# Kernel optimization log

Measured on AMD Instinct MI355X. Metric: run time of the kernel, lower is better.

The kernel has to match this reference:

```python
import jax, jax.numpy as jnp
import numpy as np

N = 100000
E = 1600000
D_IN = 128
D_HID = 128


def setup_inputs() -> dict:
    key = jax.random.key(0)
    ks = jax.random.split(key, 10)
    x = jax.random.normal(ks[0], (N, D_IN), dtype=jnp.float32)
    edge_index = jax.random.randint(ks[1], (2, E), 0, N, dtype=jnp.int64)
    def lin(k, i, o):
        kw, kb = jax.random.split(k)
        s = 1.0 / np.sqrt(i)
        return (jax.random.uniform(kw, (o, i), jnp.float32, -s, s),
                jax.random.uniform(kb, (o,), jnp.float32, -s, s))
    w0a, b0a = lin(ks[2], D_IN, D_HID)
    w0b, b0b = lin(ks[3], D_HID, D_HID)
    w1a, b1a = lin(ks[4], D_HID, D_HID)
    w1b, b1b = lin(ks[5], D_HID, D_HID)
    return {"x": x, "edge_index": edge_index,
            "w0a": w0a, "b0a": b0a, "w0b": w0b, "b0b": b0b,
            "w1a": w1a, "b1a": b1a, "w1b": w1b, "b1b": b1b}


def _gin_layer(x, src, dst, wa, ba, wb, bb):
    # GINConv, eps=0: h_i = x_i + sum_{j in N(i)} x_j (messages from src aggregated at dst)
    agg = jax.ops.segment_sum(x[src], dst, num_segments=N)  # [N, D]
    h = x + agg
    h = jax.nn.relu(h @ wa.T + ba)  # LinearBlock (no bn, no dropout)
    return h @ wb.T + bb            # final Linear of local_nn


def reference(x, edge_index, w0a, b0a, w0b, b0b, w1a, b1a, w1b, b1b):
    src, dst = edge_index[0], edge_index[1]
    h = _gin_layer(x, src, dst, w0a, b0a, w0b, b0b)
    h = _gin_layer(h, src, dst, w1a, b1a, w1b, b1b)
    return h
```

## Files before the change

### kernel.cpp

```cpp
#include <hip/hip_runtime.h>


typedef __attribute__((ext_vector_type(8))) short bf16x8;
typedef __attribute__((ext_vector_type(4))) float floatx4;

#define WS_ALIGN(x) (((x) + 255) & ~(size_t)255)
#define NBMAX 400
#define BCAP 6144

__device__ __forceinline__ unsigned short f2b(float f) {
  unsigned u = __builtin_bit_cast(unsigned, f);
  u = (u + 0x7FFF + ((u >> 16) & 1)) >> 16;
  return (unsigned short)u;
}
__device__ __forceinline__ float b2f(unsigned u16) {
  return __builtin_bit_cast(float, u16 << 16);
}

__global__ __launch_bounds__(256) void bucket_split(const int* __restrict__ src,
                                                    const int* __restrict__ dst,
                                                    int* __restrict__ bcnt,
                                                    unsigned* __restrict__ barr, int E, int nb) {
  __shared__ int cnt[NBMAX], base[NBMAX], cur[NBMAX];
  int t = threadIdx.x;
  for (int i = t; i < nb; i += 256) { cnt[i] = 0; cur[i] = 0; }
  __syncthreads();
  int e0 = blockIdx.x * 8192;
  int s[32], d[32];
#pragma unroll
  for (int k = 0; k < 32; k++) {
    int e = e0 + k * 256 + t;
    if (e < E) { s[k] = src[e]; d[k] = dst[e]; } else { d[k] = -1; }
  }
#pragma unroll
  for (int k = 0; k < 32; k++)
    if (d[k] >= 0) atomicAdd(&cnt[d[k] >> 8], 1);
  __syncthreads();
  for (int i = t; i < nb; i += 256) base[i] = cnt[i] ? atomicAdd(&bcnt[i], cnt[i]) : 0;
  __syncthreads();
#pragma unroll
  for (int k = 0; k < 32; k++)
    if (d[k] >= 0) {
      int b = d[k] >> 8;
      int r = atomicAdd(&cur[b], 1);
      barr[(size_t)b * BCAP + base[b] + r] = ((unsigned)(d[k] & 255) << 17) | (unsigned)s[k];
    }
}

__global__ void bucket_scan(const int* __restrict__ bcnt, int* __restrict__ sbase, int nb,
                            int* __restrict__ rowptr, int n) {
  __shared__ int buf[512];
  int t = threadIdx.x;
  int v = (t < nb) ? bcnt[t] : 0;
  buf[t] = v;
  __syncthreads();
  for (int off = 1; off < 512; off <<= 1) {
    int add = (t >= off) ? buf[t - off] : 0;
    __syncthreads();
    buf[t] += add;
    __syncthreads();
  }
  if (t < nb) sbase[t] = buf[t] - v;
  if (t == nb - 1) { sbase[nb] = buf[t]; rowptr[n] = buf[t]; }
}

__global__ __launch_bounds__(256) void bucket_csr(const unsigned* __restrict__ barr,
                                                  const int* __restrict__ bcnt,
                                                  const int* __restrict__ sbase,
                                                  int* __restrict__ rowptr, int* __restrict__ srt,
                                                  int n) {
  __shared__ int cnt[256], off[256], off2[256];
  int b = blockIdx.x, t = threadIdx.x;
  int cb = bcnt[b];
  int node0 = b * 256;
  int nlocal = min(256, n - node0);
  cnt[t] = 0;
  off2[t] = 0;
  __syncthreads();
  const unsigned* bp = barr + (size_t)b * BCAP;
  for (int i = t; i < cb; i += 256) atomicAdd(&cnt[bp[i] >> 17], 1);
  __syncthreads();
  int v = cnt[t];
  off[t] = v;
  __syncthreads();
  for (int o = 1; o < 256; o <<= 1) {
    int add = (t >= o) ? off[t - o] : 0;
    __syncthreads();
    off[t] += add;
    __syncthreads();
  }
  int excl = off[t] - v;
  int sb = sbase[b];
  if (t < nlocal) rowptr[node0 + t] = sb + excl;
  cnt[t] = excl;
  __syncthreads();
  for (int i = t; i < cb; i += 256) {
    unsigned pk = bp[i];
    int local = pk >> 17;
    int r = atomicAdd(&off2[local], 1);
    srt[sb + cnt[local] + r] = pk & 0x1FFFF;
  }
}

__global__ void cvt_kernel(const float* __restrict__ x, unsigned short* __restrict__ xb, int n4) {
  int i = blockIdx.x * blockDim.x + threadIdx.x;
  if (i < n4) {
    float4 v = ((const float4*)x)[i];
    uint2 pk;
    pk.x = (unsigned)f2b(v.x) | ((unsigned)f2b(v.y) << 16);
    pk.y = (unsigned)f2b(v.z) | ((unsigned)f2b(v.w) << 16);
    ((uint2*)xb)[i] = pk;
  }
}

__global__ __launch_bounds__(256) void aggregate_bf16(const unsigned short* __restrict__ X,
                                                      const int* __restrict__ rowptr,
                                                      const int* __restrict__ srt,
                                                      unsigned short* __restrict__ out, int n) {
  int w = blockIdx.x * 4 + (threadIdx.x >> 6);
  if (w >= n) return;
  int lane = threadIdx.x & 63;
  int c = lane & 15;
  int s = lane >> 4;
  const uint4* Xv = (const uint4*)X;

  float acc[8];
#pragma unroll
  for (int i = 0; i < 8; i++) acc[i] = 0.f;

  if (s == 0) {
    uint4 u = Xv[(size_t)w * 16 + c];
    acc[0] += b2f(u.x & 0xffff); acc[1] += b2f(u.x >> 16);
    acc[2] += b2f(u.y & 0xffff); acc[3] += b2f(u.y >> 16);
    acc[4] += b2f(u.z & 0xffff); acc[5] += b2f(u.z >> 16);
    acc[6] += b2f(u.w & 0xffff); acc[7] += b2f(u.w >> 16);
  }

  int p0 = rowptr[w], e = rowptr[w + 1];
  int trips = (e - p0 + 3) >> 2;
  int idx = p0 + s;
#pragma unroll 2
  for (int i = 0; i < trips; i++, idx += 4) {
    bool valid = idx < e;
    int r = srt[valid ? idx : (e - 1)];
    uint4 u = Xv[(size_t)r * 16 + c];
    if (!valid) { u.x = 0; u.y = 0; u.z = 0; u.w = 0; }
    acc[0] += b2f(u.x & 0xffff); acc[1] += b2f(u.x >> 16);
    acc[2] += b2f(u.y & 0xffff); acc[3] += b2f(u.y >> 16);
    acc[4] += b2f(u.z & 0xffff); acc[5] += b2f(u.z >> 16);
    acc[6] += b2f(u.w & 0xffff); acc[7] += b2f(u.w >> 16);
  }

#pragma unroll
  for (int i = 0; i < 8; i++) {
    acc[i] += __shfl_xor(acc[i], 16, 64);
    acc[i] += __shfl_xor(acc[i], 32, 64);
  }

  unsigned pk = (unsigned)f2b(acc[2 * s]) | ((unsigned)f2b(acc[2 * s + 1]) << 16);
  ((unsigned*)out)[(size_t)w * 64 + c * 4 + s] = pk;
}

__device__ __forceinline__ void stage_w(char* buf, const float* __restrict__ W, int t) {
  for (int idx = t; idx < 2048; idx += 512) {
    int nrow = idx >> 4, c = idx & 15;
    float4 a = ((const float4*)W)[idx * 2];
    float4 b = ((const float4*)W)[idx * 2 + 1];
    uint4 pk;
    pk.x = (unsigned)f2b(a.x) | ((unsigned)f2b(a.y) << 16);
    pk.y = (unsigned)f2b(a.z) | ((unsigned)f2b(a.w) << 16);
    pk.z = (unsigned)f2b(b.x) | ((unsigned)f2b(b.y) << 16);
    pk.w = (unsigned)f2b(b.z) | ((unsigned)f2b(b.w) << 16);
    *(uint4*)(buf + nrow * 256 + ((c ^ (nrow & 15)) << 4)) = pk;
  }
}

template <int OUT_BF16>
__global__ __launch_bounds__(512) void mlp_kernel(
    const unsigned short* __restrict__ A, const float* __restrict__ Wa,
    const float* __restrict__ ba, const float* __restrict__ Wb,
    const float* __restrict__ bb, void* __restrict__ Cout, int n) {
  __shared__ __align__(16) char lds[65536];
  char* bufA = lds;
  char* bufB = lds + 32768;
  int t = threadIdx.x;
  stage_w(bufA, Wa, t);
  stage_w(bufB, Wb, t);

  int wave = t >> 6, lane = t & 63;
  int m = lane & 15, q = lane >> 4;
  int rbase = blockIdx.x * 128;
  int rowA = rbase + wave * 16 + m;
  int rA = rowA < n ? rowA : (n - 1);

  bf16x8 af[4];
  const bf16x8* Arow = (const bf16x8*)(A + (size_t)rA * 128);
#pragma unroll
  for (int ks = 0; ks < 4; ks++) af[ks] = Arow[ks * 4 + q];

  __syncthreads();

  floatx4 acc[8];
  floatx4 zf = {0.f, 0.f, 0.f, 0.f};
#pragma unroll
  for (int j = 0; j < 8; j++) acc[j] = zf;
#pragma unroll
  for (int ks = 0; ks < 4; ks++) {
#pragma unroll
    for (int j = 0; j < 8; j++) {
      bf16x8 bf = *(const bf16x8*)(bufA + (j * 16 + m) * 256 + (((ks * 4 + q) ^ m) << 4));
      acc[j] = __builtin_amdgcn_mfma_f32_16x16x32_bf16(af[ks], bf, acc[j], 0, 0, 0);
    }
  }
  __syncthreads();

#pragma unroll
  for (int j = 0; j < 8; j++) {
    float bias = ba[j * 16 + m];
#pragma unroll
    for (int reg = 0; reg < 4; reg++) {
      float v = fmaxf(acc[j][reg] + bias, 0.f);
      int lr = wave * 16 + q * 4 + reg;
      int col = j * 16 + m;
      *(unsigned short*)(bufA + lr * 256 + (((col >> 3) ^ (lr & 15)) << 4) + (col & 7) * 2) =
          f2b(v);
    }
  }
  __syncthreads();

  int lrA = wave * 16 + m;
#pragma unroll
  for (int ks = 0; ks < 4; ks++)
    af[ks] = *(const bf16x8*)(bufA + lrA * 256 + (((ks * 4 + q) ^ m) << 4));
#pragma unroll
  for (int j = 0; j < 8; j++) acc[j] = zf;
#pragma unroll
  for (int ks = 0; ks < 4; ks++) {
#pragma unroll
    for (int j = 0; j < 8; j++) {
      bf16x8 bf = *(const bf16x8*)(bufB + (j * 16 + m) * 256 + (((ks * 4 + q) ^ m) << 4));
      acc[j] = __builtin_amdgcn_mfma_f32_16x16x32_bf16(af[ks], bf, acc[j], 0, 0, 0);
    }
  }

#pragma unroll
  for (int j = 0; j < 8; j++) {
    float bias = bb[j * 16 + m];
#pragma unroll
    for (int reg = 0; reg < 4; reg++) {
      int row = rbase + wave * 16 + q * 4 + reg;
      if (row >= n) continue;
      float v = acc[j][reg] + bias;
      int col = j * 16 + m;
      if (OUT_BF16)
        ((unsigned short*)Cout)[(size_t)row * 128 + col] = f2b(v);
      else
        ((float*)Cout)[(size_t)row * 128 + col] = v;
    }
  }
}

extern "C" void kernel_launch(void* const* d_in, const int* in_sizes, int n_in,
                              void* d_out, int out_size, void* d_ws, size_t ws_size,
                              hipStream_t stream) {
  const float* x   = (const float*)d_in[0];
  const int*   ei  = (const int*)d_in[1];
  const float* w0a = (const float*)d_in[2];
  const float* b0a = (const float*)d_in[3];
  const float* w0b = (const float*)d_in[4];
  const float* b0b = (const float*)d_in[5];
  const float* w1a = (const float*)d_in[6];
  const float* b1a = (const float*)d_in[7];
  const float* w1b = (const float*)d_in[8];
  const float* b1b = (const float*)d_in[9];
  float* out = (float*)d_out;

  int n = in_sizes[0] / 128;
  int E = in_sizes[1] / 2;
  const int* src = ei;
  const int* dst = ei + E;
  int nb = (n + 255) / 256;

  char* w = (char*)d_ws;
  int* rowptr = (int*)w;           w += WS_ALIGN((size_t)(n + 1) * 4);
  int* sbase = (int*)w;            w += WS_ALIGN((size_t)(NBMAX + 1) * 4);
  int* bcnt = (int*)w;             w += WS_ALIGN((size_t)NBMAX * 4);
  int* srt = (int*)w;              w += WS_ALIGN((size_t)E * 4);
  unsigned short* xb = (unsigned short*)w;  w += WS_ALIGN((size_t)n * 128 * 2);
  unsigned* barr = (unsigned*)w;
  unsigned short* B1 = (unsigned short*)w;

  hipMemsetAsync(bcnt, 0, (size_t)nb * 4, stream);
  bucket_split<<<(E + 8191) / 8192, 256, 0, stream>>>(src, dst, bcnt, barr, E, nb);
  bucket_scan<<<1, 512, 0, stream>>>(bcnt, sbase, nb, rowptr, n);
  bucket_csr<<<nb, 256, 0, stream>>>(barr, bcnt, sbase, rowptr, srt, n);

  cvt_kernel<<<(n * 32 + 255) / 256, 256, 0, stream>>>(x, xb, n * 32);

  int agg_grid = (n + 3) / 4;
  int mlp_grid = (n + 127) / 128;

  aggregate_bf16<<<agg_grid, 256, 0, stream>>>(xb, rowptr, srt, B1, n);
  mlp_kernel<1><<<mlp_grid, 512, 0, stream>>>(B1, w0a, b0a, w0b, b0b, xb, n);

  aggregate_bf16<<<agg_grid, 256, 0, stream>>>(xb, rowptr, srt, B1, n);
  mlp_kernel<0><<<mlp_grid, 512, 0, stream>>>(B1, w1a, b1a, w1b, b1b, out, n);
}
```

Before: 333.5 us.

## Pre-convert weights once, read B from global, and streamline CSR build and aggregation

```diff
diff --git a/kernel.cpp b/kernel.cpp
--- a/kernel.cpp
+++ b/kernel.cpp
@@ -21,29 +21,40 @@
                                                     const int* __restrict__ dst,
                                                     int* __restrict__ bcnt,
                                                     unsigned* __restrict__ barr, int E, int nb) {
-  __shared__ int cnt[NBMAX], base[NBMAX], cur[NBMAX];
+  __shared__ int cnt[NBMAX], base[NBMAX];
   int t = threadIdx.x;
-  for (int i = t; i < nb; i += 256) { cnt[i] = 0; cur[i] = 0; }
-  __syncthreads();
-  int e0 = blockIdx.x * 8192;
-  int s[32], d[32];
-#pragma unroll
-  for (int k = 0; k < 32; k++) {
-    int e = e0 + k * 256 + t;
-    if (e < E) { s[k] = src[e]; d[k] = dst[e]; } else { d[k] = -1; }
-  }
-#pragma unroll
-  for (int k = 0; k < 32; k++)
-    if (d[k] >= 0) atomicAdd(&cnt[d[k] >> 8], 1);
+  for (int i = t; i < nb; i += 256) cnt[i] = 0;
+  __syncthreads();
+  int q0 = blockIdx.x * 1024;
+  int E4 = E >> 2;
+  int s[16], d[16];
+#pragma unroll
+  for (int r = 0; r < 4; r++) {
+    int qi = q0 + r * 256 + t;
+    if (qi < E4) {
+      int4 sv = ((const int4*)src)[qi];
+      int4 dv = ((const int4*)dst)[qi];
+      s[r * 4 + 0] = sv.x; d[r * 4 + 0] = dv.x;
+      s[r * 4 + 1] = sv.y; d[r * 4 + 1] = dv.y;
+      s[r * 4 + 2] = sv.z; d[r * 4 + 2] = dv.z;
+      s[r * 4 + 3] = sv.w; d[r * 4 + 3] = dv.w;
+    } else {
+      d[r * 4 + 0] = d[r * 4 + 1] = d[r * 4 + 2] = d[r * 4 + 3] = -1;
+    }
+  }
+  int rank[16];
+#pragma unroll
+  for (int k = 0; k < 16; k++)
+    rank[k] = (d[k] >= 0) ? atomicAdd(&cnt[d[k] >> 8], 1) : 0;
   __syncthreads();
   for (int i = t; i < nb; i += 256) base[i] = cnt[i] ? atomicAdd(&bcnt[i], cnt[i]) : 0;
   __syncthreads();
 #pragma unroll
-  for (int k = 0; k < 32; k++)
+  for (int k = 0; k < 16; k++)
     if (d[k] >= 0) {
       int b = d[k] >> 8;
-      int r = atomicAdd(&cur[b], 1);
-      barr[(size_t)b * BCAP + base[b] + r] = ((unsigned)(d[k] & 255) << 17) | (unsigned)s[k];
+      barr[(size_t)b * BCAP + base[b] + rank[k]] =
+          ((unsigned)(d[k] & 255) << 17) | (unsigned)s[k];
     }
 }
 
@@ -69,16 +80,25 @@
                                                   const int* __restrict__ sbase,
                                                   int* __restrict__ rowptr, int* __restrict__ srt,
                                                   int n) {
-  __shared__ int cnt[256], off[256], off2[256];
+  __shared__ unsigned ent[BCAP];
+  __shared__ int cnt[256], off[256];
   int b = blockIdx.x, t = threadIdx.x;
   int cb = bcnt[b];
   int node0 = b * 256;
   int nlocal = min(256, n - node0);
   cnt[t] = 0;
-  off2[t] = 0;
   __syncthreads();
   const unsigned* bp = barr + (size_t)b * BCAP;
-  for (int i = t; i < cb; i += 256) atomicAdd(&cnt[bp[i] >> 17], 1);
+  int rank[24];
+  int trips = (cb + 255) >> 8;
+  for (int it = 0; it < trips; it++) {
+    int i = it * 256 + t;
+    if (i < cb) {
+      unsigned pk = bp[i];
+      ent[i] = pk;
+      rank[it] = atomicAdd(&cnt[pk >> 17], 1);
+    }
+  }
   __syncthreads();
   int v = cnt[t];
   off[t] = v;
@@ -94,11 +114,12 @@
   if (t < nlocal) rowptr[node0 + t] = sb + excl;
   cnt[t] = excl;
   __syncthreads();
-  for (int i = t; i < cb; i += 256) {
-    unsigned pk = bp[i];
-    int local = pk >> 17;
-    int r = atomicAdd(&off2[local], 1);
-    srt[sb + cnt[local] + r] = pk & 0x1FFFF;
+  for (int it = 0; it < trips; it++) {
+    int i = it * 256 + t;
+    if (i < cb) {
+      unsigned pk = ent[i];
+      srt[sb + cnt[pk >> 17] + rank[it]] = pk & 0x1FFFF;
+    }
   }
 }
 
@@ -112,6 +133,29 @@
     ((uint2*)xb)[i] = pk;
   }
 }
+
+__global__ void wcvt_kernel(const float* __restrict__ w0, const float* __restrict__ w1,
+                            const float* __restrict__ w2, const float* __restrict__ w3,
+                            uint4* __restrict__ img) {
+  const float* W = (blockIdx.y == 0) ? w0 : (blockIdx.y == 1) ? w1 : (blockIdx.y == 2) ? w2 : w3;
+  int idx = blockIdx.x * 256 + threadIdx.x;
+  float4 a = ((const float4*)W)[idx * 2];
+  float4 b = ((const float4*)W)[idx * 2 + 1];
+  uint4 pk;
+  pk.x = (unsigned)f2b(a.x) | ((unsigned)f2b(a.y) << 16);
+  pk.y = (unsigned)f2b(a.z) | ((unsigned)f2b(a.w) << 16);
+  pk.z = (unsigned)f2b(b.x) | ((unsigned)f2b(b.y) << 16);
+  pk.w = (unsigned)f2b(b.z) | ((unsigned)f2b(b.w) << 16);
+  img[(size_t)blockIdx.y * 2048 + idx] = pk;
+}
+
+#define ACC8(u)                                             \
+  do {                                                      \
+    acc[0] += b2f(u.x & 0xffff); acc[1] += b2f(u.x >> 16);  \
+    acc[2] += b2f(u.y & 0xffff); acc[3] += b2f(u.y >> 16);  \
+    acc[4] += b2f(u.z & 0xffff); acc[5] += b2f(u.z >> 16);  \
+    acc[6] += b2f(u.w & 0xffff); acc[7] += b2f(u.w >> 16);  \
+  } while (0)
 
 __global__ __launch_bounds__(256) void aggregate_bf16(const unsigned short* __restrict__ X,
                                                       const int* __restrict__ rowptr,
@@ -130,25 +174,24 @@
 
   if (s == 0) {
     uint4 u = Xv[(size_t)w * 16 + c];
-    acc[0] += b2f(u.x & 0xffff); acc[1] += b2f(u.x >> 16);
-    acc[2] += b2f(u.y & 0xffff); acc[3] += b2f(u.y >> 16);
-    acc[4] += b2f(u.z & 0xffff); acc[5] += b2f(u.z >> 16);
-    acc[6] += b2f(u.w & 0xffff); acc[7] += b2f(u.w >> 16);
+    ACC8(u);
   }
 
   int p0 = rowptr[w], e = rowptr[w + 1];
-  int trips = (e - p0 + 3) >> 2;
+  int cnt = e - p0;
+  int trips = cnt >> 2;
   int idx = p0 + s;
 #pragma unroll 2
   for (int i = 0; i < trips; i++, idx += 4) {
-    bool valid = idx < e;
-    int r = srt[valid ? idx : (e - 1)];
+    int r = __builtin_nontemporal_load(&srt[idx]);
     uint4 u = Xv[(size_t)r * 16 + c];
-    if (!valid) { u.x = 0; u.y = 0; u.z = 0; u.w = 0; }
-    acc[0] += b2f(u.x & 0xffff); acc[1] += b2f(u.x >> 16);
-    acc[2] += b2f(u.y & 0xffff); acc[3] += b2f(u.y >> 16);
-    acc[4] += b2f(u.z & 0xffff); acc[5] += b2f(u.z >> 16);
-    acc[6] += b2f(u.w & 0xffff); acc[7] += b2f(u.w >> 16);
+    ACC8(u);
+  }
+  int rem = cnt & 3;
+  if (s < rem) {
+    int r = __builtin_nontemporal_load(&srt[p0 + trips * 4 + s]);
+    uint4 u = Xv[(size_t)r * 16 + c];
+    ACC8(u);
   }
 
 #pragma unroll
@@ -156,63 +199,41 @@
     acc[i] += __shfl_xor(acc[i], 16, 64);
     acc[i] += __shfl_xor(acc[i], 32, 64);
   }
-
   unsigned pk = (unsigned)f2b(acc[2 * s]) | ((unsigned)f2b(acc[2 * s + 1]) << 16);
   ((unsigned*)out)[(size_t)w * 64 + c * 4 + s] = pk;
 }
 
-__device__ __forceinline__ void stage_w(char* buf, const float* __restrict__ W, int t) {
-  for (int idx = t; idx < 2048; idx += 512) {
-    int nrow = idx >> 4, c = idx & 15;
-    float4 a = ((const float4*)W)[idx * 2];
-    float4 b = ((const float4*)W)[idx * 2 + 1];
-    uint4 pk;
-    pk.x = (unsigned)f2b(a.x) | ((unsigned)f2b(a.y) << 16);
-    pk.y = (unsigned)f2b(a.z) | ((unsigned)f2b(a.w) << 16);
-    pk.z = (unsigned)f2b(b.x) | ((unsigned)f2b(b.y) << 16);
-    pk.w = (unsigned)f2b(b.z) | ((unsigned)f2b(b.w) << 16);
-    *(uint4*)(buf + nrow * 256 + ((c ^ (nrow & 15)) << 4)) = pk;
-  }
-}
-
 template <int OUT_BF16>
-__global__ __launch_bounds__(512) void mlp_kernel(
-    const unsigned short* __restrict__ A, const float* __restrict__ Wa,
-    const float* __restrict__ ba, const float* __restrict__ Wb,
+__global__ __launch_bounds__(256) void mlp_kernel(
+    const unsigned short* __restrict__ A, const unsigned short* __restrict__ WaI,
+    const float* __restrict__ ba, const unsigned short* __restrict__ WbI,
     const float* __restrict__ bb, void* __restrict__ Cout, int n) {
-  __shared__ __align__(16) char lds[65536];
-  char* bufA = lds;
-  char* bufB = lds + 32768;
-  int t = threadIdx.x;
-  stage_w(bufA, Wa, t);
-  stage_w(bufB, Wb, t);
-
-  int wave = t >> 6, lane = t & 63;
+  __shared__ __align__(16) char hbuf[16384];
+  int t = threadIdx.x, wave = t >> 6, lane = t & 63;
   int m = lane & 15, q = lane >> 4;
-  int rbase = blockIdx.x * 128;
-  int rowA = rbase + wave * 16 + m;
+  char* myh = hbuf + wave * 4096;
+  int r0 = (blockIdx.x * 4 + wave) * 16;
+  int rowA = r0 + m;
   int rA = rowA < n ? rowA : (n - 1);
+
+  const bf16x8* Wa = (const bf16x8*)WaI;
+  const bf16x8* Wb = (const bf16x8*)WbI;
 
   bf16x8 af[4];
   const bf16x8* Arow = (const bf16x8*)(A + (size_t)rA * 128);
 #pragma unroll
   for (int ks = 0; ks < 4; ks++) af[ks] = Arow[ks * 4 + q];
 
-  __syncthreads();
-
   floatx4 acc[8];
   floatx4 zf = {0.f, 0.f, 0.f, 0.f};
 #pragma unroll
   for (int j = 0; j < 8; j++) acc[j] = zf;
 #pragma unroll
-  for (int ks = 0; ks < 4; ks++) {
-#pragma unroll
-    for (int j = 0; j < 8; j++) {
-      bf16x8 bf = *(const bf16x8*)(bufA + (j * 16 + m) * 256 + (((ks * 4 + q) ^ m) << 4));
-      acc[j] = __builtin_amdgcn_mfma_f32_16x16x32_bf16(af[ks], bf, acc[j], 0, 0, 0);
-    }
-  }
-  __syncthreads();
+  for (int ks = 0; ks < 4; ks++)
+#pragma unroll
+    for (int j = 0; j < 8; j++)
+      acc[j] = __builtin_amdgcn_mfma_f32_16x16x32_bf16(af[ks], Wa[j * 256 + m * 16 + ks * 4 + q],
+                                                       acc[j], 0, 0, 0);
 
 #pragma unroll
   for (int j = 0; j < 8; j++) {
@@ -220,35 +241,30 @@
 #pragma unroll
     for (int reg = 0; reg < 4; reg++) {
       float v = fmaxf(acc[j][reg] + bias, 0.f);
-      int lr = wave * 16 + q * 4 + reg;
+      int lr = q * 4 + reg;
       int col = j * 16 + m;
-      *(unsigned short*)(bufA + lr * 256 + (((col >> 3) ^ (lr & 15)) << 4) + (col & 7) * 2) =
-          f2b(v);
-    }
-  }
-  __syncthreads();
-
-  int lrA = wave * 16 + m;
+      *(unsigned short*)(myh + lr * 256 + (((col >> 3) ^ lr) << 4) + (col & 7) * 2) = f2b(v);
+    }
+  }
+
 #pragma unroll
   for (int ks = 0; ks < 4; ks++)
-    af[ks] = *(const bf16x8*)(bufA + lrA * 256 + (((ks * 4 + q) ^ m) << 4));
+    af[ks] = *(const bf16x8*)(myh + m * 256 + (((ks * 4 + q) ^ m) << 4));
 #pragma unroll
   for (int j = 0; j < 8; j++) acc[j] = zf;
 #pragma unroll
-  for (int ks = 0; ks < 4; ks++) {
-#pragma unroll
-    for (int j = 0; j < 8; j++) {
-      bf16x8 bf = *(const bf16x8*)(bufB + (j * 16 + m) * 256 + (((ks * 4 + q) ^ m) << 4));
-      acc[j] = __builtin_amdgcn_mfma_f32_16x16x32_bf16(af[ks], bf, acc[j], 0, 0, 0);
-    }
-  }
+  for (int ks = 0; ks < 4; ks++)
+#pragma unroll
+    for (int j = 0; j < 8; j++)
+      acc[j] = __builtin_amdgcn_mfma_f32_16x16x32_bf16(af[ks], Wb[j * 256 + m * 16 + ks * 4 + q],
+                                                       acc[j], 0, 0, 0);
 
 #pragma unroll
   for (int j = 0; j < 8; j++) {
     float bias = bb[j * 16 + m];
 #pragma unroll
     for (int reg = 0; reg < 4; reg++) {
-      int row = rbase + wave * 16 + q * 4 + reg;
+      int row = r0 + q * 4 + reg;
       if (row >= n) continue;
       float v = acc[j][reg] + bias;
       int col = j * 16 + m;
@@ -287,22 +303,26 @@
   int* bcnt = (int*)w;             w += WS_ALIGN((size_t)NBMAX * 4);
   int* srt = (int*)w;              w += WS_ALIGN((size_t)E * 4);
   unsigned short* xb = (unsigned short*)w;  w += WS_ALIGN((size_t)n * 128 * 2);
+  uint4* wimg = (uint4*)w;         w += WS_ALIGN((size_t)4 * 32768);
   unsigned* barr = (unsigned*)w;
   unsigned short* B1 = (unsigned short*)w;
 
+  wcvt_kernel<<<dim3(8, 4), 256, 0, stream>>>(w0a, w0b, w1a, w1b, wimg);
+
   hipMemsetAsync(bcnt, 0, (size_t)nb * 4, stream);
-  bucket_split<<<(E + 8191) / 8192, 256, 0, stream>>>(src, dst, bcnt, barr, E, nb);
+  bucket_split<<<(E + 4095) / 4096, 256, 0, stream>>>(src, dst, bcnt, barr, E, nb);
   bucket_scan<<<1, 512, 0, stream>>>(bcnt, sbase, nb, rowptr, n);
   bucket_csr<<<nb, 256, 0, stream>>>(barr, bcnt, sbase, rowptr, srt, n);
 
   cvt_kernel<<<(n * 32 + 255) / 256, 256, 0, stream>>>(x, xb, n * 32);
 
   int agg_grid = (n + 3) / 4;
-  int mlp_grid = (n + 127) / 128;
-
+  int mlp_grid = (n + 63) / 64;
+
+  const unsigned short* wi = (const unsigned short*)wimg;
   aggregate_bf16<<<agg_grid, 256, 0, stream>>>(xb, rowptr, srt, B1, n);
-  mlp_kernel<1><<<mlp_grid, 512, 0, stream>>>(B1, w0a, b0a, w0b, b0b, xb, n);
+  mlp_kernel<1><<<mlp_grid, 256, 0, stream>>>(B1, wi, b0a, wi + 16384, b0b, xb, n);
 
   aggregate_bf16<<<agg_grid, 256, 0, stream>>>(xb, rowptr, srt, B1, n);
-  mlp_kernel<0><<<mlp_grid, 512, 0, stream>>>(B1, w1a, b1a, w1b, b1b, out, n);
-}
+  mlp_kernel<0><<<mlp_grid, 256, 0, stream>>>(B1, wi + 32768, b1a, wi + 49152, b1b, out, n);
+}
```

New measurement: 426.4 us. 1.28x slower.
